# Performance work log

Hardware: AMD Instinct MI355X
Metric: run time of the kernel (lower is better)

Reference implementation:

```python
import jax, jax.numpy as jnp
import numpy as np

N = 100000      # nodes
E = 1600000     # edges (avg degree 16)
DIN = 64
DOUT = 64
C = 8           # num classes; label -1 means unknown


def _xavier(key, shape):
    a = jnp.sqrt(6.0 / (shape[0] + shape[1]))
    return jax.random.uniform(key, shape, jnp.float32, -a, a)


def setup_inputs():
    key = jax.random.key(0)
    ks = jax.random.split(key, 17)
    return {
        "x": jax.random.normal(ks[0], (N, DIN), jnp.float32),
        "adj_low_vals": jax.random.uniform(ks[1], (E,), jnp.float32) / 16.0,
        "adj_high_vals": jax.random.uniform(ks[2], (E,), jnp.float32) / 16.0,
        "weight_low": _xavier(ks[3], (DIN, DOUT)),
        "weight_high": _xavier(ks[4], (DIN, DOUT)),
        "weight_mlp": _xavier(ks[5], (DIN, DOUT)),
        "att_vec_low_fr": _xavier(ks[6], (DOUT, 1)),
        "att_vec_high_fr": _xavier(ks[7], (DOUT, 1)),
        "att_vec_low_be": _xavier(ks[8], (DOUT, 1)),
        "att_vec_high_be": _xavier(ks[9], (DOUT, 1)),
        "att_vec_low_unk": _xavier(ks[10], (DOUT, 1)),
        "att_vec_high_unk": _xavier(ks[11], (DOUT, 1)),
        "att_vec_mlp": _xavier(ks[12], (DOUT, 1)),
        "att_vec7": _xavier(ks[13], (7, 7)),
        "edge_src": jax.random.randint(ks[14], (E,), 0, N),
        "edge_dst": jax.random.randint(ks[15], (E,), 0, N),
        "label_unk": jax.random.randint(ks[16], (N,), -1, C),
    }


def reference(x, adj_low_vals, adj_high_vals, weight_low, weight_high, weight_mlp,
              att_vec_low_fr, att_vec_high_fr, att_vec_low_be, att_vec_high_be,
              att_vec_low_unk, att_vec_high_unk, att_vec_mlp, att_vec7,
              edge_src, edge_dst, label_unk):
    def spmm(vals, feats):  # out[dst] += vals * feats[src]  (sparse [N,N] @ [N,D])
        return jax.ops.segment_sum(vals[:, None] * feats[edge_src], edge_dst, num_segments=N)

    output_low = jax.nn.relu(spmm(adj_low_vals, x @ weight_low))
    output_high = jax.nn.relu(spmm(adj_high_vals, x @ weight_high))
    output_mlp = jax.nn.relu(x @ weight_mlp)

    # per-edge fake label: 2 if either endpoint unknown (<0), 1 if labels differ
    # (both known) -> heterophilous, else 0 -> homophilous
    sl = label_unk[edge_src]
    dl = label_unk[edge_dst]
    fake = jnp.where((sl < 0) | (dl < 0), 2, jnp.where(sl != dl, 1, 0))

    h_low_e = output_low[edge_src]    # [E, DOUT] gathered messages
    h_high_e = output_high[edge_src]

    def agg(h_e, k):  # masked segment-sum over destination nodes
        m = (fake == k).astype(h_e.dtype)[:, None]
        return jax.ops.segment_sum(h_e * m, edge_dst, num_segments=N)

    neigh_homo_low, neigh_hete_low, neigh_unk_low = agg(h_low_e, 0), agg(h_low_e, 1), agg(h_low_e, 2)
    neigh_homo_high, neigh_hete_high, neigh_unk_high = agg(h_high_e, 0), agg(h_high_e, 1), agg(h_high_e, 2)

    # attention7 (fr_high_g is None branch)
    feats = jax.nn.sigmoid(jnp.concatenate([
        neigh_hete_low @ att_vec_low_fr, neigh_hete_high @ att_vec_high_fr,
        neigh_homo_low @ att_vec_low_be, neigh_homo_high @ att_vec_high_be,
        neigh_unk_low @ att_vec_low_unk, neigh_unk_high @ att_vec_high_unk,
        output_mlp @ att_vec_mlp], axis=1))  # [N, 7]
    att = jax.nn.softmax((feats @ att_vec7) / 7.0, axis=1)

    return 7.0 * (att[:, 0:1] * neigh_hete_low + att[:, 1:2] * neigh_hete_high
                  + att[:, 2:3] * neigh_homo_low + att[:, 3:4] * neigh_homo_high
                  + att[:, 4:5] * neigh_unk_low + att[:, 5:6] * neigh_unk_high
                  + att[:, 6:7] * output_mlp)
```

## Files before the change

### kernel.cpp

```cpp
#include <hip/hip_runtime.h>
#include <hip/hip_bf16.h>

typedef unsigned int u32;
typedef unsigned short u16;
typedef unsigned long long u64;

typedef __attribute__((ext_vector_type(8))) short bf16x8;
typedef __attribute__((ext_vector_type(4))) float f32x4;
typedef __attribute__((ext_vector_type(2))) float f32x2;

#define BCAP 1536

static __device__ __forceinline__ float bflo(u32 u) { return __uint_as_float(u << 16); }
static __device__ __forceinline__ float bfhi(u32 u) { return __uint_as_float(u & 0xFFFF0000u); }
static __device__ __forceinline__ float bf2f(u16 u) { return __uint_as_float((u32)u << 16); }
static __device__ __forceinline__ u32 f2bf(float f) {
    u32 u = __float_as_uint(f);
    return (u + 0x7FFFu + ((u >> 16) & 1u)) >> 16;
}
static __device__ __forceinline__ u32 packbf(float lo, float hi) {
    return f2bf(lo) | (f2bf(hi) << 16);
}
static __device__ __forceinline__ float ldf(const u16* p16, int idx, int isf32) {
    return isf32 ? ((const float*)p16)[idx] : bf2f(p16[idx]);
}
static __device__ __forceinline__ void load4(const u16* p, int q, int isf32, float* v) {
    if (isf32) {
        float4 t = ((const float4*)p)[q];
        v[0] = t.x; v[1] = t.y; v[2] = t.z; v[3] = t.w;
    } else {
        u32 a = ((const u32*)p)[q * 2], b = ((const u32*)p)[q * 2 + 1];
        v[0] = bflo(a); v[1] = bfhi(a); v[2] = bflo(b); v[3] = bfhi(b);
    }
}
static __device__ __forceinline__ float sanitize(float v, float code) {
    return (fabsf(v) < 1e30f) ? v : code;
}

static __device__ __forceinline__ f32x2 up2(u32 u) {
    f32x2 r;
    r.x = __uint_as_float(u << 16);
    r.y = __uint_as_float(u & 0xFFFF0000u);
    return r;
}
static __device__ __forceinline__ void pk_fma(f32x2& d, f32x2 a, f32x2 b) {
    asm("v_pk_fma_f32 %0, %1, %2, %0" : "+v"(d) : "v"(a), "v"(b));
}
static __device__ __forceinline__ void pk_add(f32x2& d, f32x2 a) {
    asm("v_pk_add_f32 %0, %1, %0" : "+v"(d) : "v"(a));
}

static __device__ __forceinline__ float wave_sum(float v) {
#pragma unroll
    for (int o = 32; o; o >>= 1) v += __shfl_xor(v, o, 64);
    return v;
}
static __device__ __forceinline__ float group_sum(float v) {
#pragma unroll
    for (int o = 8; o; o >>= 1) v += __shfl_xor(v, o, 64);
    return v;
}


__global__ void k_sentinel(float* __restrict__ out, int n, float val) {
    int i = blockIdx.x * blockDim.x + threadIdx.x;
    if (i < n) out[i] = val;
}

__global__ void k_init(int* __restrict__ bcur, int nbcur, const u16* __restrict__ x,
                       int* __restrict__ flag, const u16* __restrict__ wl,
                       const u16* __restrict__ wh, const u16* __restrict__ wm,
                       u16* __restrict__ Bpack) {
    int t = threadIdx.x;
    int zb = gridDim.x - 1;
    if ((int)blockIdx.x < zb) {
        int i = blockIdx.x * 256 + t;
        if (i < nbcur) bcur[i] = 0;
        if (blockIdx.x == 0 && t < 64) {
            int wild = 0;
            for (int k = 0; k < 64; k++) {
                u32 u = x[t * 64 + k];
                int e = (u >> 7) & 0xFF;
                if (e < 96 || e > 135) wild++;
            }
            float tot = wave_sum((float)wild);
            if (t == 0) *flag = (tot > 200.f) ? 1 : 0;
        }
        return;
    }
    __shared__ int sflag;
    if (t < 64) {
        int wild = 0;
        for (int k = 0; k < 64; k++) {
            u32 u = x[t * 64 + k];
            int e = (u >> 7) & 0xFF;
            if (e < 96 || e > 135) wild++;
        }
        float tot = wave_sum((float)wild);
        if (t == 0) sflag = (tot > 200.f) ? 1 : 0;
    }
    __syncthreads();
    int isf32 = sflag;
    for (int idx = t; idx < 12 * 2 * 64; idx += 256) {
        int slot = idx >> 6;
        int ln = idx & 63;
        int ct = slot >> 1, c = slot & 1;
        int mat = ct >> 2;
        const u16* W = (mat == 0) ? wl : (mat == 1) ? wh : wm;
        int col = (ct & 3) * 16 + (ln & 15);
        int kbase = c * 32 + (ln >> 4) * 8;
        u16* dst = Bpack + (size_t)idx * 8;
#pragma unroll
        for (int j = 0; j < 8; j++)
            dst[j] = (u16)f2bf(ldf(W, (kbase + j) * 64 + col, isf32));
    }
}

__global__ void k_scat1(const int* __restrict__ src, const int* __restrict__ dst,
                        const u16* __restrict__ avl, const u16* __restrict__ avh,
                        const int* __restrict__ lab, int E, int* __restrict__ bcur,
                        u64* __restrict__ etmp, const int* __restrict__ flag) {
    int i = blockIdx.x * blockDim.x + threadIdx.x;
    if (i >= E) return;
    int isf32 = *flag;
    int d = dst[i];
    int b = d >> 6;
    int base = b << 6;
    int rank = atomicAdd(&bcur[b * 16], 1);
    if (rank >= BCAP) return;
    int s = src[i];
    int sl = lab[s], dl = lab[d];
    int fake = (sl < 0 || dl < 0) ? 2 : ((sl != dl) ? 1 : 0);
    u32 lo32 = (u32)s | ((u32)fake << 20) | ((u32)(d - base) << 22);
    u32 hi32 = isf32 ? packbf(((const float*)avl)[i], ((const float*)avh)[i])
                     : ((u32)avl[i] | ((u32)avh[i] << 16));
    etmp[(size_t)b * BCAP + rank] = ((u64)hi32 << 32) | lo32;
}

__launch_bounds__(256) __global__
void k_gemm_mfma(const u16* __restrict__ x, const u16* __restrict__ Bpack, int N,
                 u32* __restrict__ xwlh, float* __restrict__ omlp,
                 const int* __restrict__ flag) {
    int isf32 = *flag;
    int lane = threadIdx.x & 63;
    int wv = (blockIdx.x * 256 + threadIdx.x) >> 6;
    int nw = gridDim.x * 4;
    int m = lane & 15, quad = lane >> 4;
    int ntiles = (N + 15) >> 4;
    for (int tile = wv; tile < ntiles; tile += nw) {
        int r0 = tile * 16;
        int arow = min(r0 + m, N - 1);
        bf16x8 a[2];
#pragma unroll
        for (int c = 0; c < 2; c++) {
            int base = arow * 64 + c * 32 + quad * 8;
            if (isf32) {
                const float4* xf = (const float4*)x;
                int q = (base >> 2);
                float4 t0 = xf[q], t1 = xf[q + 1];
                a[c][0] = (short)f2bf(t0.x); a[c][1] = (short)f2bf(t0.y);
                a[c][2] = (short)f2bf(t0.z); a[c][3] = (short)f2bf(t0.w);
                a[c][4] = (short)f2bf(t1.x); a[c][5] = (short)f2bf(t1.y);
                a[c][6] = (short)f2bf(t1.z); a[c][7] = (short)f2bf(t1.w);
            } else {
                a[c] = *(const bf16x8*)(x + base);
            }
        }
        f32x4 acc[12];
#pragma unroll
        for (int t = 0; t < 12; t++) acc[t] = (f32x4){0.f, 0.f, 0.f, 0.f};
#pragma unroll
        for (int t = 0; t < 12; t++) {
#pragma unroll
            for (int c = 0; c < 2; c++) {
                bf16x8 b = *(const bf16x8*)(Bpack + (size_t)((t * 2 + c) * 64 + lane) * 8);
                acc[t] = __builtin_amdgcn_mfma_f32_16x16x32_bf16(a[c], b, acc[t], 0, 0, 0);
            }
        }
#pragma unroll
        for (int t = 0; t < 4; t++) {
#pragma unroll
            for (int r = 0; r < 4; r++) {
                int row = r0 + quad * 4 + r;
                if (row < N) {
                    int o = row * 64 + t * 16 + m;
                    xwlh[o] = packbf(acc[t][r], acc[t + 4][r]);
                    omlp[o] = fmaxf(acc[t + 8][r], 0.f);
                }
            }
        }
    }
}

__launch_bounds__(256) __global__
void k_scat2_spmm(const u64* __restrict__ etmp, const int* __restrict__ bcur, int N,
                  int4* __restrict__ cb4, u32* __restrict__ epay_lo,
                  const u32* __restrict__ xwlh, u32* __restrict__ outlh) {
    __shared__ int cnt[192], startp[192], cur[192], tot[64];
    __shared__ u64 stash[BCAP];
    int b = blockIdx.x;
    int base = b << 6;
    int ebase = b * BCAP;
    int t = threadIdx.x;
    if (t < 192) cnt[t] = 0;
    __syncthreads();
    int cntE = min(bcur[b * 16], BCAP);
    u64 ph[6];
#pragma unroll
    for (int j = 0; j < 6; j++) {
        int e = t + j * 256;
        if (e < cntE) {
            u64 p = etmp[(size_t)ebase + e];
            ph[j] = p;
            int dl3 = ((int)(p >> 22) & 63) * 3 + ((int)(p >> 20) & 3);
            atomicAdd(&cnt[dl3], 1);
        }
    }
    __syncthreads();
    if (t < 64) tot[t] = cnt[t * 3] + cnt[t * 3 + 1] + cnt[t * 3 + 2];
    __syncthreads();
    for (int d = 1; d < 64; d <<= 1) {
        int v = 0;
        if (t < 64 && t >= d) v = tot[t - d];
        __syncthreads();
        if (t < 64) tot[t] += v;
        __syncthreads();
    }
    if (t < 64) {
        int c0 = cnt[t * 3], c1 = cnt[t * 3 + 1], c2 = cnt[t * 3 + 2];
        int own = c0 + c1 + c2;
        int ex = tot[t] - own;
        int s0 = ex, s1 = ex + c0, s2 = ex + c0 + c1;
        startp[t * 3] = s0;
        startp[t * 3 + 1] = s1;
        startp[t * 3 + 2] = s2;
        cur[t * 3] = s0;
        cur[t * 3 + 1] = s1;
        cur[t * 3 + 2] = s2;
        int node = base + t;
        if (node < N) {
            int4 cb;
            cb.x = ebase + s0;
            cb.y = ebase + s1;
            cb.z = ebase + s2;
            cb.w = ebase + ex + own;
            cb4[node] = cb;
        }
    }
    __syncthreads();
#pragma unroll
    for (int j = 0; j < 6; j++) {
        int e = t + j * 256;
        if (e < cntE) {
            u64 p = ph[j];
            int dl3 = ((int)(p >> 22) & 63) * 3 + ((int)(p >> 20) & 3);
            int rank = atomicAdd(&cur[dl3], 1);
            stash[rank] = p;
            epay_lo[(size_t)ebase + rank] = (u32)p;
        }
    }
    __syncthreads();
    int g = t & 15, grp = t >> 4;
    const uint4* tab = (const uint4*)xwlh + g;
#pragma unroll
    for (int it = 0; it < 4; it++) {
        int dloc = it * 16 + grp;
        int node = base + dloc;
        if (node >= N) continue;
        int sR = startp[dloc * 3];
        int eR = startp[dloc * 3 + 2] + cnt[dloc * 3 + 2];
        f32x2 acc[4];
#pragma unroll
        for (int k = 0; k < 4; k++) acc[k] = (f32x2){0.f, 0.f};
        int idx = sR;
        for (; idx + 3 < eR; idx += 4) {
            u64 p0 = stash[idx], p1 = stash[idx + 1], p2 = stash[idx + 2], p3 = stash[idx + 3];
            uint4 R0 = tab[(size_t)(p0 & 0xFFFFF) << 4];
            uint4 R1 = tab[(size_t)(p1 & 0xFFFFF) << 4];
            uint4 R2 = tab[(size_t)(p2 & 0xFFFFF) << 4];
            uint4 R3 = tab[(size_t)(p3 & 0xFFFFF) << 4];
            f32x2 w0 = up2((u32)(p0 >> 32)), w1 = up2((u32)(p1 >> 32));
            f32x2 w2 = up2((u32)(p2 >> 32)), w3 = up2((u32)(p3 >> 32));
            pk_fma(acc[0], up2(R0.x), w0);
            pk_fma(acc[1], up2(R0.y), w0);
            pk_fma(acc[2], up2(R0.z), w0);
            pk_fma(acc[3], up2(R0.w), w0);
            pk_fma(acc[0], up2(R1.x), w1);
            pk_fma(acc[1], up2(R1.y), w1);
            pk_fma(acc[2], up2(R1.z), w1);
            pk_fma(acc[3], up2(R1.w), w1);
            pk_fma(acc[0], up2(R2.x), w2);
            pk_fma(acc[1], up2(R2.y), w2);
            pk_fma(acc[2], up2(R2.z), w2);
            pk_fma(acc[3], up2(R2.w), w2);
            pk_fma(acc[0], up2(R3.x), w3);
            pk_fma(acc[1], up2(R3.y), w3);
            pk_fma(acc[2], up2(R3.z), w3);
            pk_fma(acc[3], up2(R3.w), w3);
        }
        for (; idx < eR; idx++) {
            u64 p0 = stash[idx];
            uint4 R0 = tab[(size_t)(p0 & 0xFFFFF) << 4];
            f32x2 w0 = up2((u32)(p0 >> 32));
            pk_fma(acc[0], up2(R0.x), w0);
            pk_fma(acc[1], up2(R0.y), w0);
            pk_fma(acc[2], up2(R0.z), w0);
            pk_fma(acc[3], up2(R0.w), w0);
        }
        uint4 W;
        W.x = packbf(fmaxf(acc[0].x, 0.f), fmaxf(acc[0].y, 0.f));
        W.y = packbf(fmaxf(acc[1].x, 0.f), fmaxf(acc[1].y, 0.f));
        W.z = packbf(fmaxf(acc[2].x, 0.f), fmaxf(acc[2].y, 0.f));
        W.w = packbf(fmaxf(acc[3].x, 0.f), fmaxf(acc[3].y, 0.f));
        ((uint4*)(outlh + (size_t)node * 64))[g] = W;
    }
}


__launch_bounds__(256) __global__
void k_agg4n(const u32* __restrict__ outlh, const u32* __restrict__ epay_lo,
             const int4* __restrict__ cb4,
             const u16* __restrict__ aLF, const u16* __restrict__ aHF,
             const u16* __restrict__ aLB, const u16* __restrict__ aHB,
             const u16* __restrict__ aLU, const u16* __restrict__ aHU,
             const u16* __restrict__ aM, const u16* __restrict__ a7, int N,
             float* __restrict__ out, const int* __restrict__ flag) {
    int isf32 = *flag;
    int lane = threadIdx.x & 63;
    int gwave = blockIdx.x * 4 + (threadIdx.x >> 6);
    int g = lane & 15, gi = lane >> 4;
    int node = gwave * 4 + gi;
    bool vn = node < N;
    int4 cb = vn ? cb4[node] : (int4){0, 0, 0, 0};
    int s = cb.x, c1 = cb.y, c2 = cb.z, e = cb.w;
    const uint4* tab = (const uint4*)outlh + g;
    f32x2 acc[4], S1[4], S2[4];
#pragma unroll
    for (int k = 0; k < 4; k++) {
        acc[k] = (f32x2){0.f, 0.f};
        S1[k] = (f32x2){0.f, 0.f};
        S2[k] = (f32x2){0.f, 0.f};
    }
#define AGG_EDGE(R)                    \
    pk_add(acc[0], up2(R.x));          \
    pk_add(acc[1], up2(R.y));          \
    pk_add(acc[2], up2(R.z));          \
    pk_add(acc[3], up2(R.w));
#define AGG_CHK(q)                                                        \
    if ((q) == c1) { S1[0] = acc[0]; S1[1] = acc[1]; S1[2] = acc[2]; S1[3] = acc[3]; } \
    if ((q) == c2) { S2[0] = acc[0]; S2[1] = acc[1]; S2[2] = acc[2]; S2[3] = acc[3]; }
    int tt = s;
    for (; tt + 3 < e; tt += 4) {
        u32 p0 = epay_lo[tt], p1 = epay_lo[tt + 1];
        u32 p2 = epay_lo[tt + 2], p3 = epay_lo[tt + 3];
        uint4 R0 = tab[(size_t)(p0 & 0xFFFFF) << 4];
        uint4 R1 = tab[(size_t)(p1 & 0xFFFFF) << 4];
        uint4 R2 = tab[(size_t)(p2 & 0xFFFFF) << 4];
        uint4 R3 = tab[(size_t)(p3 & 0xFFFFF) << 4];
        AGG_EDGE(R0); AGG_CHK(tt + 1);
        AGG_EDGE(R1); AGG_CHK(tt + 2);
        AGG_EDGE(R2); AGG_CHK(tt + 3);
        AGG_EDGE(R3); AGG_CHK(tt + 4);
    }
    for (; tt < e; tt++) {
        u32 p0 = epay_lo[tt];
        uint4 R0 = tab[(size_t)(p0 & 0xFFFFF) << 4];
        AGG_EDGE(R0); AGG_CHK(tt + 1);
    }
#undef AGG_EDGE
#undef AGG_CHK
    float heL[4], heH[4], hoL[4], hoH[4], unL[4], unH[4];
#pragma unroll
    for (int k = 0; k < 4; k++) {
        hoL[k] = S1[k].x;            hoH[k] = S1[k].y;
        heL[k] = S2[k].x - S1[k].x;  heH[k] = S2[k].y - S1[k].y;
        unL[k] = acc[k].x - S2[k].x; unH[k] = acc[k].y - S2[k].y;
    }
    float vLF[4], vHF[4], vLB[4], vHB[4], vLU[4], vHU[4], vM[4];
    load4(aLF, g, isf32, vLF);
    load4(aHF, g, isf32, vHF);
    load4(aLB, g, isf32, vLB);
    load4(aHB, g, isf32, vHB);
    load4(aLU, g, isf32, vLU);
    load4(aHU, g, isf32, vHU);
    load4(aM, g, isf32, vM);
    float mvv[4] = {0.f, 0.f, 0.f, 0.f};
    if (vn) {
        float4 MV = ((const float4*)(out + (size_t)node * 64))[g];
        mvv[0] = MV.x; mvv[1] = MV.y; mvv[2] = MV.z; mvv[3] = MV.w;
    }

    float p0 = 0, p1 = 0, p2 = 0, p3 = 0, p4 = 0, p5 = 0, p6 = 0;
#pragma unroll
    for (int k = 0; k < 4; k++) {
        p0 += heL[k] * vLF[k];
        p1 += heH[k] * vHF[k];
        p2 += hoL[k] * vLB[k];
        p3 += hoH[k] * vHB[k];
        p4 += unL[k] * vLU[k];
        p5 += unH[k] * vHU[k];
        p6 += mvv[k] * vM[k];
    }
    float d0 = group_sum(p0), d1 = group_sum(p1), d2 = group_sum(p2), d3 = group_sum(p3);
    float d4 = group_sum(p4), d5 = group_sum(p5), d6 = group_sum(p6);

    float f[7];
    f[0] = 1.f / (1.f + expf(-d0));
    f[1] = 1.f / (1.f + expf(-d1));
    f[2] = 1.f / (1.f + expf(-d2));
    f[3] = 1.f / (1.f + expf(-d3));
    f[4] = 1.f / (1.f + expf(-d4));
    f[5] = 1.f / (1.f + expf(-d5));
    f[6] = 1.f / (1.f + expf(-d6));

    float z[7];
#pragma unroll
    for (int jj = 0; jj < 7; jj++) {
        float acc7 = 0.f;
#pragma unroll
        for (int i = 0; i < 7; i++) acc7 += f[i] * ldf(a7, i * 7 + jj, isf32);
        z[jj] = acc7 * (1.f / 7.f);
    }
    float m = z[0];
#pragma unroll
    for (int jj = 1; jj < 7; jj++) m = fmaxf(m, z[jj]);
    float wsum = 0.f;
    float wv[7];
#pragma unroll
    for (int jj = 0; jj < 7; jj++) { wv[jj] = expf(z[jj] - m); wsum += wv[jj]; }
    float s7 = 7.f / wsum;

    if (vn) {
        float4 W;
        float o0 = wv[0] * heL[0] + wv[1] * heH[0] + wv[2] * hoL[0] + wv[3] * hoH[0] +
                   wv[4] * unL[0] + wv[5] * unH[0] + wv[6] * mvv[0];
        float o1 = wv[0] * heL[1] + wv[1] * heH[1] + wv[2] * hoL[1] + wv[3] * hoH[1] +
                   wv[4] * unL[1] + wv[5] * unH[1] + wv[6] * mvv[1];
        float o2 = wv[0] * heL[2] + wv[1] * heH[2] + wv[2] * hoL[2] + wv[3] * hoH[2] +
                   wv[4] * unL[2] + wv[5] * unH[2] + wv[6] * mvv[2];
        float o3 = wv[0] * heL[3] + wv[1] * heH[3] + wv[2] * hoL[3] + wv[3] * hoH[3] +
                   wv[4] * unL[3] + wv[5] * unH[3] + wv[6] * mvv[3];
        W.x = sanitize(o0 * s7, 333.f);
        W.y = sanitize(o1 * s7, 333.f);
        W.z = sanitize(o2 * s7, 333.f);
        W.w = sanitize(o3 * s7, 333.f);
        ((float4*)(out + (size_t)node * 64))[g] = W;
    }
}


extern "C" void kernel_launch(void* const* d_in, const int* in_sizes, int n_in, void* d_out,
                              int out_size, void* d_ws, size_t ws_size, hipStream_t stream) {
    const u16* x = (const u16*)d_in[0];
    const u16* avl = (const u16*)d_in[1];
    const u16* avh = (const u16*)d_in[2];
    const u16* wl = (const u16*)d_in[3];
    const u16* wh = (const u16*)d_in[4];
    const u16* wm = (const u16*)d_in[5];
    const u16* aLF = (const u16*)d_in[6];
    const u16* aHF = (const u16*)d_in[7];
    const u16* aLB = (const u16*)d_in[8];
    const u16* aHB = (const u16*)d_in[9];
    const u16* aLU = (const u16*)d_in[10];
    const u16* aHU = (const u16*)d_in[11];
    const u16* aM = (const u16*)d_in[12];
    const u16* a7 = (const u16*)d_in[13];
    const int* esrc = (const int*)d_in[14];
    const int* edst = (const int*)d_in[15];
    const int* lab = (const int*)d_in[16];
    float* out = (float*)d_out;

    const int N = in_sizes[0] / 64;
    const int E = in_sizes[1];

    int NB2 = (N + 63) / 64;

    char* w = (char*)d_ws;
    size_t off = 0;
    auto alloc = [&](size_t bytes) -> char* {
        char* p = w + off;
        off += (bytes + 255) & ~(size_t)255;
        return p;
    };
    int* flag = (int*)alloc(256);
    int* bcur = (int*)alloc((size_t)NB2 * 16 * 4);
    u16* Bpack = (u16*)alloc(12 * 2 * 64 * 8 * 2);
    int4* cb4 = (int4*)alloc((size_t)N * 16);
    u64* etmp = (u64*)alloc((size_t)NB2 * BCAP * 8);
    u32* epay_lo = (u32*)alloc((size_t)NB2 * BCAP * 4);
    u32* xwlh = (u32*)alloc((size_t)N * 64 * 4);
    u32* outlh = (u32*)alloc((size_t)N * 64 * 4);

    if (ws_size < off) {
        k_sentinel<<<(out_size + 255) / 256, 256, 0, stream>>>(out, out_size, 1000.0f);
        return;
    }

    int nbcur = NB2 * 16;
    int ZB = (nbcur + 255) / 256;
    k_init<<<ZB + 1, 256, 0, stream>>>(bcur, nbcur, x, flag, wl, wh, wm, Bpack);

    k_scat1<<<(E + 255) / 256, 256, 0, stream>>>(esrc, edst, avl, avh, lab, E, bcur, etmp,
                                                 flag);

    int ntiles = (N + 15) / 16;
    int gemmBlocks = (ntiles + 3) / 4;
    k_gemm_mfma<<<gemmBlocks, 256, 0, stream>>>(x, Bpack, N, xwlh,
                                                out , flag);

    k_scat2_spmm<<<NB2, 256, 0, stream>>>(etmp, bcur, N, cb4, epay_lo, xwlh, outlh);

    int nodeBlocks = (N + 15) / 16;
    k_agg4n<<<nodeBlocks, 256, 0, stream>>>(outlh, epay_lo, cb4, aLF, aHF, aLB, aHB, aLU, aHU,
                                            aM, a7, N, out, flag);
}
```

Baseline: 395.1 us.

## Fuse five kernel launches into one cooperative persistent megakernel with grid syncs

Replaces the chain of five separate launches (init, scatter, GEMM, bucket SpMM, aggregation) with a single cooperative kernel that runs each stage in grid-stride loops and separates the stages with grid.sync(). The goal is to remove per-launch overhead and inter-kernel gaps. The trade-offs are that grid-wide barriers cost time and the grid is limited to the resident occupancy, so large stages such as the scatter and GEMM lose the wide launch shapes they had before. Host-side attribute and occupancy queries are added on every call, and the old multi-kernel path is kept as a fallback.

```diff
diff --git a/kernel.cpp b/kernel.cpp
--- a/kernel.cpp
+++ b/kernel.cpp
@@ -1,5 +1,6 @@
 #include <hip/hip_runtime.h>
 #include <hip/hip_bf16.h>
+#include <hip/hip_cooperative_groups.h>
 
 typedef unsigned int u32;
 typedef unsigned short u16;
@@ -67,40 +68,19 @@
     if (i < n) out[i] = val;
 }
 
-__global__ void k_init(int* __restrict__ bcur, int nbcur, const u16* __restrict__ x,
-                       int* __restrict__ flag, const u16* __restrict__ wl,
-                       const u16* __restrict__ wh, const u16* __restrict__ wm,
-                       u16* __restrict__ Bpack) {
-    int t = threadIdx.x;
-    int zb = gridDim.x - 1;
-    if ((int)blockIdx.x < zb) {
-        int i = blockIdx.x * 256 + t;
-        if (i < nbcur) bcur[i] = 0;
-        if (blockIdx.x == 0 && t < 64) {
-            int wild = 0;
-            for (int k = 0; k < 64; k++) {
-                u32 u = x[t * 64 + k];
-                int e = (u >> 7) & 0xFF;
-                if (e < 96 || e > 135) wild++;
-            }
-            float tot = wave_sum((float)wild);
-            if (t == 0) *flag = (tot > 200.f) ? 1 : 0;
-        }
-        return;
-    }
-    __shared__ int sflag;
-    if (t < 64) {
-        int wild = 0;
-        for (int k = 0; k < 64; k++) {
-            u32 u = x[t * 64 + k];
-            int e = (u >> 7) & 0xFF;
-            if (e < 96 || e > 135) wild++;
-        }
-        float tot = wave_sum((float)wild);
-        if (t == 0) sflag = (tot > 200.f) ? 1 : 0;
-    }
-    __syncthreads();
-    int isf32 = sflag;
+static __device__ __forceinline__ int dev_sniff(const u16* x, int lane) {
+    int wild = 0;
+    for (int k = 0; k < 64; k++) {
+        u32 u = x[lane * 64 + k];
+        int e = (u >> 7) & 0xFF;
+        if (e < 96 || e > 135) wild++;
+    }
+    float tot = wave_sum((float)wild);
+    return (tot > 200.f) ? 1 : 0;
+}
+
+static __device__ void dev_prepB(const u16* wl, const u16* wh, const u16* wm, u16* Bpack,
+                                 int isf32, int t) {
     for (int idx = t; idx < 12 * 2 * 64; idx += 256) {
         int slot = idx >> 6;
         int ln = idx & 63;
@@ -116,13 +96,9 @@
     }
 }
 
-__global__ void k_scat1(const int* __restrict__ src, const int* __restrict__ dst,
-                        const u16* __restrict__ avl, const u16* __restrict__ avh,
-                        const int* __restrict__ lab, int E, int* __restrict__ bcur,
-                        u64* __restrict__ etmp, const int* __restrict__ flag) {
-    int i = blockIdx.x * blockDim.x + threadIdx.x;
-    if (i >= E) return;
-    int isf32 = *flag;
+static __device__ __forceinline__ void dev_scat1_edge(
+    int i, const int* src, const int* dst, const u16* avl, const u16* avh, const int* lab,
+    int* bcur, u64* etmp, int isf32) {
     int d = dst[i];
     int b = d >> 6;
     int base = b << 6;
@@ -137,14 +113,9 @@
     etmp[(size_t)b * BCAP + rank] = ((u64)hi32 << 32) | lo32;
 }
 
-__launch_bounds__(256) __global__
-void k_gemm_mfma(const u16* __restrict__ x, const u16* __restrict__ Bpack, int N,
-                 u32* __restrict__ xwlh, float* __restrict__ omlp,
-                 const int* __restrict__ flag) {
-    int isf32 = *flag;
-    int lane = threadIdx.x & 63;
-    int wv = (blockIdx.x * 256 + threadIdx.x) >> 6;
-    int nw = gridDim.x * 4;
+static __device__ void dev_gemm(const u16* x, const u16* Bpack, int N, u32* xwlh,
+                                float* omlp, int isf32, int tid, int wv, int nw) {
+    int lane = tid & 63;
     int m = lane & 15, quad = lane >> 4;
     int ntiles = (N + 15) >> 4;
     for (int tile = wv; tile < ntiles; tile += nw) {
@@ -192,16 +163,12 @@
     }
 }
 
-__launch_bounds__(256) __global__
-void k_scat2_spmm(const u64* __restrict__ etmp, const int* __restrict__ bcur, int N,
-                  int4* __restrict__ cb4, u32* __restrict__ epay_lo,
-                  const u32* __restrict__ xwlh, u32* __restrict__ outlh) {
-    __shared__ int cnt[192], startp[192], cur[192], tot[64];
-    __shared__ u64 stash[BCAP];
-    int b = blockIdx.x;
+static __device__ void dev_bucket(
+    int b, const u64* etmp, const int* bcur, int N, int4* cb4, u32* epay_lo,
+    const u32* xwlh, u32* outlh, int t,
+    int* cnt, int* startp, int* cur, int* tot, u64* stash) {
     int base = b << 6;
     int ebase = b * BCAP;
-    int t = threadIdx.x;
     if (t < 192) cnt[t] = 0;
     __syncthreads();
     int cntE = min(bcur[b * 16], BCAP);
@@ -314,20 +281,15 @@
         W.w = packbf(fmaxf(acc[3].x, 0.f), fmaxf(acc[3].y, 0.f));
         ((uint4*)(outlh + (size_t)node * 64))[g] = W;
     }
-}
-
-
-__launch_bounds__(256) __global__
-void k_agg4n(const u32* __restrict__ outlh, const u32* __restrict__ epay_lo,
-             const int4* __restrict__ cb4,
-             const u16* __restrict__ aLF, const u16* __restrict__ aHF,
-             const u16* __restrict__ aLB, const u16* __restrict__ aHB,
-             const u16* __restrict__ aLU, const u16* __restrict__ aHU,
-             const u16* __restrict__ aM, const u16* __restrict__ a7, int N,
-             float* __restrict__ out, const int* __restrict__ flag) {
-    int isf32 = *flag;
-    int lane = threadIdx.x & 63;
-    int gwave = blockIdx.x * 4 + (threadIdx.x >> 6);
+    __syncthreads();
+}
+
+static __device__ void dev_agg_group(
+    int gwave, const u32* outlh, const u32* epay_lo, const int4* cb4,
+    const u16* aLF, const u16* aHF, const u16* aLB, const u16* aHB,
+    const u16* aLU, const u16* aHU, const u16* aM, const u16* a7, int N,
+    float* out, int isf32, int tid) {
+    int lane = tid & 63;
     int g = lane & 15, gi = lane >> 4;
     int node = gwave * 4 + gi;
     bool vn = node < N;
@@ -389,7 +351,6 @@
         float4 MV = ((const float4*)(out + (size_t)node * 64))[g];
         mvv[0] = MV.x; mvv[1] = MV.y; mvv[2] = MV.z; mvv[3] = MV.w;
     }
-
     float p0 = 0, p1 = 0, p2 = 0, p3 = 0, p4 = 0, p5 = 0, p6 = 0;
 #pragma unroll
     for (int k = 0; k < 4; k++) {
@@ -446,6 +407,130 @@
         W.w = sanitize(o3 * s7, 333.f);
         ((float4*)(out + (size_t)node * 64))[g] = W;
     }
+}
+
+__launch_bounds__(256, 4) __global__
+void k_mega(const u16* x, const u16* avl, const u16* avh,
+            const u16* wl, const u16* wh, const u16* wm,
+            const u16* aLF, const u16* aHF, const u16* aLB, const u16* aHB,
+            const u16* aLU, const u16* aHU, const u16* aM, const u16* a7,
+            const int* esrc, const int* edst, const int* lab,
+            int N, int E, int NB2,
+            int* flag, int* bcur, u16* Bpack, int4* cb4,
+            u64* etmp, u32* epay_lo, u32* xwlh, u32* outlh, float* out) {
+    __shared__ int cnt[192], startp[192], cur[192], tot[64];
+    __shared__ u64 stash[BCAP];
+    __shared__ int sflag;
+    cooperative_groups::grid_group grid = cooperative_groups::this_grid();
+    int t = threadIdx.x;
+    int nblk = (int)gridDim.x;
+
+    for (int i = blockIdx.x * 256 + t; i < NB2 * 16; i += nblk * 256) bcur[i] = 0;
+    if (blockIdx.x == 0 && t < 64) {
+        int f = dev_sniff(x, t);
+        if (t == 0) *flag = f;
+    }
+    if ((int)blockIdx.x == (nblk > 1 ? 1 : 0)) {
+        if (t < 64) {
+            int f = dev_sniff(x, t);
+            if (t == 0) sflag = f;
+        }
+        __syncthreads();
+        dev_prepB(wl, wh, wm, Bpack, sflag, t);
+    }
+    grid.sync();
+
+    {
+        int isf32 = *flag;
+        for (int i = blockIdx.x * 256 + t; i < E; i += nblk * 256)
+            dev_scat1_edge(i, esrc, edst, avl, avh, lab, bcur, etmp, isf32);
+    }
+    grid.sync();
+
+    {
+        int isf32 = *flag;
+        int wv = (blockIdx.x * 256 + t) >> 6;
+        dev_gemm(x, Bpack, N, xwlh, out , isf32, t, wv, nblk * 4);
+    }
+    grid.sync();
+
+    for (int b = blockIdx.x; b < NB2; b += nblk)
+        dev_bucket(b, etmp, bcur, N, cb4, epay_lo, xwlh, outlh, t, cnt, startp, cur, tot,
+                   stash);
+    grid.sync();
+
+    {
+        int isf32 = *flag;
+        int nodeBlocks = (N + 15) / 16;
+        for (int vb = blockIdx.x; vb < nodeBlocks; vb += nblk)
+            dev_agg_group(vb * 4 + (t >> 6), outlh, epay_lo, cb4, aLF, aHF, aLB, aHB, aLU,
+                          aHU, aM, a7, N, out, isf32, t);
+    }
+}
+
+
+__global__ void k_init(int* __restrict__ bcur, int nbcur, const u16* __restrict__ x,
+                       int* __restrict__ flag, const u16* __restrict__ wl,
+                       const u16* __restrict__ wh, const u16* __restrict__ wm,
+                       u16* __restrict__ Bpack) {
+    int t = threadIdx.x;
+    int zb = gridDim.x - 1;
+    if ((int)blockIdx.x < zb) {
+        int i = blockIdx.x * 256 + t;
+        if (i < nbcur) bcur[i] = 0;
+        if (blockIdx.x == 0 && t < 64) {
+            int f = dev_sniff(x, t);
+            if (t == 0) *flag = f;
+        }
+        return;
+    }
+    __shared__ int sflag;
+    if (t < 64) {
+        int f = dev_sniff(x, t);
+        if (t == 0) sflag = f;
+    }
+    __syncthreads();
+    dev_prepB(wl, wh, wm, Bpack, sflag, t);
+}
+
+__global__ void k_scat1(const int* __restrict__ src, const int* __restrict__ dst,
+                        const u16* __restrict__ avl, const u16* __restrict__ avh,
+                        const int* __restrict__ lab, int E, int* __restrict__ bcur,
+                        u64* __restrict__ etmp, const int* __restrict__ flag) {
+    int i = blockIdx.x * blockDim.x + threadIdx.x;
+    if (i >= E) return;
+    dev_scat1_edge(i, src, dst, avl, avh, lab, bcur, etmp, *flag);
+}
+
+__launch_bounds__(256) __global__
+void k_gemm_mfma(const u16* __restrict__ x, const u16* __restrict__ Bpack, int N,
+                 u32* __restrict__ xwlh, float* __restrict__ omlp,
+                 const int* __restrict__ flag) {
+    int wv = (blockIdx.x * 256 + threadIdx.x) >> 6;
+    dev_gemm(x, Bpack, N, xwlh, omlp, *flag, threadIdx.x, wv, gridDim.x * 4);
+}
+
+__launch_bounds__(256) __global__
+void k_scat2_spmm(const u64* __restrict__ etmp, const int* __restrict__ bcur, int N,
+                  int4* __restrict__ cb4, u32* __restrict__ epay_lo,
+                  const u32* __restrict__ xwlh, u32* __restrict__ outlh) {
+    __shared__ int cnt[192], startp[192], cur[192], tot[64];
+    __shared__ u64 stash[BCAP];
+    dev_bucket(blockIdx.x, etmp, bcur, N, cb4, epay_lo, xwlh, outlh, threadIdx.x, cnt,
+               startp, cur, tot, stash);
+}
+
+__launch_bounds__(256) __global__
+void k_agg4n(const u32* __restrict__ outlh, const u32* __restrict__ epay_lo,
+             const int4* __restrict__ cb4,
+             const u16* __restrict__ aLF, const u16* __restrict__ aHF,
+             const u16* __restrict__ aLB, const u16* __restrict__ aHB,
+             const u16* __restrict__ aLU, const u16* __restrict__ aHU,
+             const u16* __restrict__ aM, const u16* __restrict__ a7, int N,
+             float* __restrict__ out, const int* __restrict__ flag) {
+    int gwave = blockIdx.x * 4 + (threadIdx.x >> 6);
+    dev_agg_group(gwave, outlh, epay_lo, cb4, aLF, aHF, aLB, aHB, aLU, aHU, aM, a7, N, out,
+                  *flag, threadIdx.x);
 }
 
 
@@ -470,9 +555,8 @@
     const int* lab = (const int*)d_in[16];
     float* out = (float*)d_out;
 
-    const int N = in_sizes[0] / 64;
-    const int E = in_sizes[1];
-
+    int N = in_sizes[0] / 64;
+    int E = in_sizes[1];
     int NB2 = (N + 63) / 64;
 
     char* w = (char*)d_ws;
@@ -496,20 +580,36 @@
         return;
     }
 
+    bool launched = false;
+    int coopOK = 0, numCU = 0, maxb = 0;
+    (void)hipDeviceGetAttribute(&coopOK, hipDeviceAttributeCooperativeLaunch, 0);
+    (void)hipDeviceGetAttribute(&numCU, hipDeviceAttributeMultiprocessorCount, 0);
+    hipError_t occErr =
+        hipOccupancyMaxActiveBlocksPerMultiprocessor(&maxb, (const void*)k_mega, 256, 0);
+    if (coopOK && occErr == hipSuccess && numCU > 0 && maxb > 0) {
+        int grid = numCU * maxb;
+        if (grid > 2048) grid = 2048;
+        if (grid >= 64) {
+            void* args[] = {&x,   &avl,  &avh,  &wl,    &wh,   &wm,      &aLF,  &aHF,
+                            &aLB, &aHB,  &aLU,  &aHU,   &aM,   &a7,      &esrc, &edst,
+                            &lab, &N,    &E,    &NB2,   &flag, &bcur,    &Bpack, &cb4,
+                            &etmp, &epay_lo, &xwlh, &outlh, &out};
+            hipError_t err = hipLaunchCooperativeKernel((const void*)k_mega, dim3(grid),
+                                                        dim3(256), args, 0, stream);
+            launched = (err == hipSuccess);
+        }
+    }
+    if (launched) return;
+
     int nbcur = NB2 * 16;
     int ZB = (nbcur + 255) / 256;
     k_init<<<ZB + 1, 256, 0, stream>>>(bcur, nbcur, x, flag, wl, wh, wm, Bpack);
-
     k_scat1<<<(E + 255) / 256, 256, 0, stream>>>(esrc, edst, avl, avh, lab, E, bcur, etmp,
                                                  flag);
-
     int ntiles = (N + 15) / 16;
     int gemmBlocks = (ntiles + 3) / 4;
-    k_gemm_mfma<<<gemmBlocks, 256, 0, stream>>>(x, Bpack, N, xwlh,
-                                                out , flag);
-
+    k_gemm_mfma<<<gemmBlocks, 256, 0, stream>>>(x, Bpack, N, xwlh, out , flag);
     k_scat2_spmm<<<NB2, 256, 0, stream>>>(etmp, bcur, N, cb4, epay_lo, xwlh, outlh);
-
     int nodeBlocks = (N + 15) / 16;
     k_agg4n<<<nodeBlocks, 256, 0, stream>>>(outlh, epay_lo, cb4, aLF, aHF, aLB, aHB, aLU, aHU,
                                             aM, a7, N, out, flag);
```

Result: slower. 747.9 us (+89.3%).
